# Kernel tuning notes

Measured on AMD Instinct MI355X. Metric: run time of the kernel, lower is better.

The kernel has to match this reference:

```python
import jax, jax.numpy as jnp
import numpy as np

LN_EPS = 1e-5


def setup_inputs() -> dict:
    key = jax.random.key(0)
    k1, k2, k3 = jax.random.split(key, 3)
    B, C, N, T, K = 8, 64, 512, 288, 32
    x = jax.random.normal(k1, (B, C, N, T), dtype=jnp.float32)
    HEs = jax.random.uniform(k2, (N, K), dtype=jnp.float32)  # relu(tanh(...)) in [0,1)
    edge_map = jax.random.normal(k3, (K, K), dtype=jnp.float32) / np.sqrt(K)
    return {"x": x, "HEs": HEs, "edge_map": edge_map}


def reference(x, HEs, edge_map):
    # x: [B, C, N, T]; HEs: [N, K]; edge_map: [K, K]
    B, C, N, T = x.shape
    xt = jnp.transpose(x, (0, 3, 2, 1))            # [B, T, N, C]
    feat = xt.reshape(B * T, N, C)                 # [B*T, N, C]
    # hyperedge aggregation: HEs^T @ feat
    hyper_feat = jnp.einsum('nk,bnc->bkc', HEs, feat)          # [B*T, K, C]
    hyper_mapped = jax.nn.relu(jnp.einsum('kj,bjc->bkc', edge_map, hyper_feat))
    hyper_out = hyper_mapped + hyper_feat
    # scatter back to nodes
    y = jax.nn.relu(jnp.einsum('nk,bkc->bnc', HEs, hyper_out)) # [B*T, N, C]
    y = y.reshape(B, T, N, C)
    z = y + xt
    # fresh LayerNorm over last dim (C), affine params are identity (ones/zeros)
    mu = jnp.mean(z, axis=-1, keepdims=True)
    var = jnp.mean(jnp.square(z - mu), axis=-1, keepdims=True)
    z = (z - mu) * jax.lax.rsqrt(var + LN_EPS)
    return jnp.transpose(z, (0, 3, 2, 1))          # [B, C, N, T]
```

## Files before the change

kernel.cpp:

```cpp
#include <hip/hip_runtime.h>

#define B_ 8
#define C_ 64
#define N_ 512
#define T_ 288
#define K_ 32

typedef __bf16 bf16;
typedef __attribute__((ext_vector_type(4))) __bf16 bf16x4;
typedef __attribute__((ext_vector_type(8))) __bf16 bf16x8;
typedef __attribute__((ext_vector_type(4))) float f32x4;

__global__ __launch_bounds__(256) void k_prep(const void* __restrict__ x,
                                              const void* __restrict__ hes,
                                              const void* __restrict__ em,
                                              bf16* __restrict__ hesb,
                                              bf16* __restrict__ hest,
                                              bf16* __restrict__ emb,
                                              int* __restrict__ flag) {
    __shared__ float sm[256];
    const bf16* xb = (const bf16*)x;
    float m = 0.f;
    for (int i = threadIdx.x; i < 4096; i += 256) {
        float a = fabsf((float)xb[i]);
        if (!(a <= 1000.f)) a = 1e30f;
        m = fmaxf(m, a);
    }
    sm[threadIdx.x] = m;
    __syncthreads();
    for (int s = 128; s > 0; s >>= 1) {
        if (threadIdx.x < s) sm[threadIdx.x] = fmaxf(sm[threadIdx.x], sm[threadIdx.x + s]);
        __syncthreads();
    }
    const int f32 = (sm[0] > 1000.f) ? 1 : 0;
    if (blockIdx.x == 0 && threadIdx.x == 0) *flag = f32;

    int idx = blockIdx.x * 256 + threadIdx.x;
    if (idx < N_ * K_) {
        float v = f32 ? ((const float*)hes)[idx] : (float)((const bf16*)hes)[idx];
        hesb[idx] = (bf16)v;
        int n = idx >> 5, k = idx & 31;
        hest[k * N_ + n] = (bf16)v;
    }
    if (idx < K_ * K_) {
        float v = f32 ? ((const float*)em)[idx] : (float)((const bf16*)em)[idx];
        emb[idx] = (bf16)v;
    }
}

template <int F32>
__device__ __forceinline__ void hyper_body(const void* __restrict__ x,
                                           const bf16* __restrict__ hest,
                                           const bf16* __restrict__ emb,
                                           bf16* __restrict__ ho) {
    const int tile = blockIdx.x, c = blockIdx.y, b = blockIdx.z;
    const int lane = threadIdx.x;
    const int col  = lane & 15;
    const int q    = lane >> 4;
    const int t0   = tile * 32;
    const size_t xbase = ((size_t)(b * C_ + c)) * N_ * T_;

    __shared__ bf16  xT[32][136];
    __shared__ float hf[K_][33];

    const int tq = lane & 7;
    const int rw = lane >> 3;

    f32x4 acc[2][2] = {};
    for (int chunk = 0; chunk < 4; ++chunk) {
        const int nc = chunk * 128;
        #pragma unroll
        for (int it = 0; it < 16; ++it) {
            const int row = it * 8 + rw;
            const size_t gi = xbase + (size_t)(nc + row) * T_ + t0 + 4 * tq;
            float v0, v1, v2, v3;
            if (F32) {
                f32x4 v = *(const f32x4*)((const float*)x + gi);
                v0 = v[0]; v1 = v[1]; v2 = v[2]; v3 = v[3];
            } else {
                bf16x4 v = *(const bf16x4*)((const bf16*)x + gi);
                v0 = (float)v[0]; v1 = (float)v[1]; v2 = (float)v[2]; v3 = (float)v[3];
            }
            xT[4 * tq + 0][row] = (bf16)v0;
            xT[4 * tq + 1][row] = (bf16)v1;
            xT[4 * tq + 2][row] = (bf16)v2;
            xT[4 * tq + 3][row] = (bf16)v3;
        }
        __syncthreads();
        #pragma unroll
        for (int s = 0; s < 4; ++s) {
            const int nl = s * 32;
            const int ng = nc + nl;
            bf16x8 a0 = *(const bf16x8*)(hest + (size_t)(col) * N_ + ng + 8 * q);
            bf16x8 a1 = *(const bf16x8*)(hest + (size_t)(16 + col) * N_ + ng + 8 * q);
            bf16x8 b0 = *(const bf16x8*)(&xT[col][nl + 8 * q]);
            bf16x8 b1 = *(const bf16x8*)(&xT[16 + col][nl + 8 * q]);
            acc[0][0] = __builtin_amdgcn_mfma_f32_16x16x32_bf16(a0, b0, acc[0][0], 0, 0, 0);
            acc[0][1] = __builtin_amdgcn_mfma_f32_16x16x32_bf16(a0, b1, acc[0][1], 0, 0, 0);
            acc[1][0] = __builtin_amdgcn_mfma_f32_16x16x32_bf16(a1, b0, acc[1][0], 0, 0, 0);
            acc[1][1] = __builtin_amdgcn_mfma_f32_16x16x32_bf16(a1, b1, acc[1][1], 0, 0, 0);
        }
        __syncthreads();
    }

    #pragma unroll
    for (int mt = 0; mt < 2; ++mt)
        #pragma unroll
        for (int tt = 0; tt < 2; ++tt)
            #pragma unroll
            for (int r = 0; r < 4; ++r)
                hf[16 * mt + 4 * q + r][16 * tt + col] = acc[mt][tt][r];
    __syncthreads();

    f32x4 acc2[2][2];
    #pragma unroll
    for (int mt = 0; mt < 2; ++mt) {
        bf16x8 a = *(const bf16x8*)(emb + (size_t)(16 * mt + col) * K_ + 8 * q);
        #pragma unroll
        for (int tt = 0; tt < 2; ++tt) {
            bf16x8 bb;
            #pragma unroll
            for (int jj = 0; jj < 8; ++jj)
                bb[jj] = (bf16)hf[8 * q + jj][16 * tt + col];
            f32x4 zero = {};
            acc2[mt][tt] = __builtin_amdgcn_mfma_f32_16x16x32_bf16(a, bb, zero, 0, 0, 0);
        }
    }

    #pragma unroll
    for (int mt = 0; mt < 2; ++mt)
        #pragma unroll
        for (int tt = 0; tt < 2; ++tt) {
            bf16x4 v;
            #pragma unroll
            for (int r = 0; r < 4; ++r) {
                float hv = acc2[mt][tt][r];
                hv = hv > 0.f ? hv : 0.f;
                hv += acc[mt][tt][r];
                v[r] = (bf16)hv;
            }
            *(bf16x4*)(ho + (((size_t)(b * C_ + c)) * T_ + t0 + 16 * tt + col) * K_
                          + 16 * mt + 4 * q) = v;
        }
}

__global__ __launch_bounds__(64, 3) void k_hyper(const void* __restrict__ x,
                                                 const int* __restrict__ flag,
                                                 const bf16* __restrict__ hest,
                                                 const bf16* __restrict__ emb,
                                                 bf16* __restrict__ ho) {
    if (*flag) hyper_body<1>(x, hest, emb, ho);
    else       hyper_body<0>(x, hest, emb, ho);
}

template <int F32>
__device__ __forceinline__ void scatter_body(const void* __restrict__ x,
                                             const bf16* __restrict__ hesb,
                                             const bf16* __restrict__ ho,
                                             void* __restrict__ outp) {
    const int wg  = blockIdx.x;
    const int b   = wg & 7;
    const int pos = wg >> 3;
    const int bx  = pos % 9;
    const int n0  = (pos / 9) * 16;

    const int tid   = threadIdx.x;
    const int w     = tid >> 6;
    const int lane  = tid & 63;
    const int col   = lane & 15;
    const int q     = lane >> 4;
    const int thalf = w & 1;
    const int cgrp  = w >> 1;
    const int t0    = bx * 32 + thalf * 16;

    bf16x8 hb = *(const bf16x8*)(hesb + (size_t)(n0 + col) * K_ + 8 * q);

    f32x4 z[16];
    float s1[4] = {0.f, 0.f, 0.f, 0.f}, s2[4] = {0.f, 0.f, 0.f, 0.f};
    const bf16* hob = ho + (((size_t)(b * C_)) * T_ + t0 + col) * K_ + 8 * q;
    const size_t xb = ((size_t)b * C_) * (size_t)N_ * T_;
    #pragma unroll
    for (int i = 0; i < 16; ++i) {
        const int c = cgrp * 16 + i;
        bf16x8 a = *(const bf16x8*)(hob + (size_t)c * T_ * K_);
        f32x4 zero = {};
        f32x4 zz = __builtin_amdgcn_mfma_f32_16x16x32_bf16(a, hb, zero, 0, 0, 0);
        const size_t xi = xb + ((size_t)c * N_ + n0 + col) * T_ + t0 + 4 * q;
        f32x4 xv;
        if (F32) {
            xv = *(const f32x4*)((const float*)x + xi);
        } else {
            bf16x4 x4 = *(const bf16x4*)((const bf16*)x + xi);
            xv[0] = (float)x4[0]; xv[1] = (float)x4[1];
            xv[2] = (float)x4[2]; xv[3] = (float)x4[3];
        }
        #pragma unroll
        for (int r = 0; r < 4; ++r) {
            float v = zz[r];
            v = v > 0.f ? v : 0.f;
            v += xv[r];
            zz[r] = v;
            s1[r] += v;
            s2[r] += v * v;
        }
        z[i] = zz;
    }

    __shared__ float sh1[2][4][16][17];
    __shared__ float sh2[2][4][16][17];
    #pragma unroll
    for (int r = 0; r < 4; ++r) {
        sh1[thalf][cgrp][4 * q + r][col] = s1[r];
        sh2[thalf][cgrp][4 * q + r][col] = s2[r];
    }
    __syncthreads();

    {
        const int th = tid >> 8, rr = (tid >> 4) & 15, cc = tid & 15;
        float S1 = sh1[th][0][rr][cc] + sh1[th][1][rr][cc]
                 + sh1[th][2][rr][cc] + sh1[th][3][rr][cc];
        float S2 = sh2[th][0][rr][cc] + sh2[th][1][rr][cc]
                 + sh2[th][2][rr][cc] + sh2[th][3][rr][cc];
        float mu  = S1 * (1.f / 64.f);
        float var = S2 * (1.f / 64.f) - mu * mu;
        float rs  = rsqrtf(var + 1e-5f);
        sh1[th][0][rr][cc] = mu;
        sh2[th][0][rr][cc] = rs;
    }
    __syncthreads();

    float mu_r[4], rs_r[4];
    #pragma unroll
    for (int r = 0; r < 4; ++r) {
        mu_r[r] = sh1[thalf][0][4 * q + r][col];
        rs_r[r] = sh2[thalf][0][4 * q + r][col];
    }
    #pragma unroll
    for (int i = 0; i < 16; ++i) {
        const int c = cgrp * 16 + i;
        const size_t oi = ((size_t)(b * C_ + c) * N_ + n0 + col) * T_ + t0 + 4 * q;
        if (F32) {
            f32x4 v;
            #pragma unroll
            for (int r = 0; r < 4; ++r) v[r] = (z[i][r] - mu_r[r]) * rs_r[r];
            *(f32x4*)((float*)outp + oi) = v;
        } else {
            bf16x4 v;
            #pragma unroll
            for (int r = 0; r < 4; ++r) v[r] = (bf16)((z[i][r] - mu_r[r]) * rs_r[r]);
            *(bf16x4*)((bf16*)outp + oi) = v;
        }
    }
}

__global__ __launch_bounds__(512, 2) void k_scatter_ln(const void* __restrict__ x,
                                                       const int* __restrict__ flag,
                                                       const bf16* __restrict__ hesb,
                                                       const bf16* __restrict__ ho,
                                                       void* __restrict__ outp) {
    if (*flag) scatter_body<1>(x, hesb, ho, outp);
    else       scatter_body<0>(x, hesb, ho, outp);
}

extern "C" void kernel_launch(void* const* d_in, const int* in_sizes, int n_in,
                              void* d_out, int out_size, void* d_ws, size_t ws_size,
                              hipStream_t stream) {
    const void* x   = d_in[0];
    const void* hes = d_in[1];
    const void* em  = d_in[2];

    char* ws = (char*)d_ws;
    int*  flag = (int*)ws;
    bf16* hesb = (bf16*)(ws + 64);
    bf16* hest = hesb + (size_t)N_ * K_;
    bf16* emb  = hest + (size_t)K_ * N_;
    bf16* ho   = emb  + (size_t)K_ * K_;

    k_prep<<<dim3((N_ * K_ + 255) / 256), 256, 0, stream>>>(x, hes, em, hesb, hest, emb, flag);
    k_hyper<<<dim3(T_ / 32, C_, B_), 64, 0, stream>>>(x, flag, hest, emb, ho);
    k_scatter_ln<<<dim3((T_ / 32) * (N_ / 16) * B_, 1, 1), 512, 0, stream>>>(x, flag, hesb, ho, d_out);
}
```

Before: 603.1 us.

## Rework hyper-kernel x staging, alias LDS buffers, add nontemporal IO and raise occupancy

The hyper kernel now loads x with lanes mapped to consecutive time steps. Each lane reads four node rows as scalar loads and writes a packed bf16x4 into the transposed LDS tile, replacing the old scattered per-element LDS stores. The xT and hf shared buffers are aliased to cut LDS use, and both kernels raise their launch-bounds occupancy hints. The scatter/LayerNorm kernel switches to nontemporal loads of x and nontemporal output stores. The risks are scalar global loads being less efficient than vector loads, and register pressure from the higher occupancy hint on the 512-thread kernel, which holds 16 f32x4 values per thread.

```diff
diff --git a/kernel.cpp b/kernel.cpp
--- a/kernel.cpp
+++ b/kernel.cpp
@@ -60,39 +60,37 @@
     const int t0   = tile * 32;
     const size_t xbase = ((size_t)(b * C_ + c)) * N_ * T_;
 
-    __shared__ bf16  xT[32][136];
-    __shared__ float hf[K_][33];
-
-    const int tq = lane & 7;
-    const int rw = lane >> 3;
+    __shared__ char smraw[32 * 136 * sizeof(bf16)];
+    bf16 (*xT)[136] = (bf16(*)[136])smraw;
+    float (*hf)[33] = (float(*)[33])smraw;
+
+    const int tcol = lane & 31;
+    const int ng   = lane >> 5;
 
     f32x4 acc[2][2] = {};
     for (int chunk = 0; chunk < 4; ++chunk) {
         const int nc = chunk * 128;
         #pragma unroll
-        for (int it = 0; it < 16; ++it) {
-            const int row = it * 8 + rw;
-            const size_t gi = xbase + (size_t)(nc + row) * T_ + t0 + 4 * tq;
-            float v0, v1, v2, v3;
-            if (F32) {
-                f32x4 v = *(const f32x4*)((const float*)x + gi);
-                v0 = v[0]; v1 = v[1]; v2 = v[2]; v3 = v[3];
-            } else {
-                bf16x4 v = *(const bf16x4*)((const bf16*)x + gi);
-                v0 = (float)v[0]; v1 = (float)v[1]; v2 = (float)v[2]; v3 = (float)v[3];
+        for (int a = 0; a < 16; ++a) {
+            const int nb = a * 8 + ng * 4;
+            const size_t gi = xbase + (size_t)(nc + nb) * T_ + t0 + tcol;
+            bf16x4 w;
+            #pragma unroll
+            for (int j = 0; j < 4; ++j) {
+                float v;
+                if (F32) v = ((const float*)x)[gi + (size_t)j * T_];
+                else     v = (float)((const bf16*)x)[gi + (size_t)j * T_];
+                w[j] = (bf16)v;
             }
-            xT[4 * tq + 0][row] = (bf16)v0;
-            xT[4 * tq + 1][row] = (bf16)v1;
-            xT[4 * tq + 2][row] = (bf16)v2;
-            xT[4 * tq + 3][row] = (bf16)v3;
+            *(bf16x4*)(&xT[tcol][nb]) = w;
         }
         __syncthreads();
         #pragma unroll
         for (int s = 0; s < 4; ++s) {
             const int nl = s * 32;
-            const int ng = nc + nl;
-            bf16x8 a0 = *(const bf16x8*)(hest + (size_t)(col) * N_ + ng + 8 * q);
-            bf16x8 a1 = *(const bf16x8*)(hest + (size_t)(16 + col) * N_ + ng + 8 * q);
+            const int ng2 = nc + nl;
+            bf16x8 a0 = *(const bf16x8*)(hest + (size_t)(col) * N_ + ng2 + 8 * q);
+            bf16x8 a1 = *(const bf16x8*)(hest + (size_t)(16 + col) * N_ + ng2 + 8 * q);
             bf16x8 b0 = *(const bf16x8*)(&xT[col][nl + 8 * q]);
             bf16x8 b1 = *(const bf16x8*)(&xT[16 + col][nl + 8 * q]);
             acc[0][0] = __builtin_amdgcn_mfma_f32_16x16x32_bf16(a0, b0, acc[0][0], 0, 0, 0);
@@ -144,7 +142,7 @@
         }
 }
 
-__global__ __launch_bounds__(64, 3) void k_hyper(const void* __restrict__ x,
+__global__ __launch_bounds__(64, 4) void k_hyper(const void* __restrict__ x,
                                                  const int* __restrict__ flag,
                                                  const bf16* __restrict__ hest,
                                                  const bf16* __restrict__ emb,
@@ -188,9 +186,9 @@
         const size_t xi = xb + ((size_t)c * N_ + n0 + col) * T_ + t0 + 4 * q;
         f32x4 xv;
         if (F32) {
-            xv = *(const f32x4*)((const float*)x + xi);
+            xv = __builtin_nontemporal_load((const f32x4*)((const float*)x + xi));
         } else {
-            bf16x4 x4 = *(const bf16x4*)((const bf16*)x + xi);
+            bf16x4 x4 = __builtin_nontemporal_load((const bf16x4*)((const bf16*)x + xi));
             xv[0] = (float)x4[0]; xv[1] = (float)x4[1];
             xv[2] = (float)x4[2]; xv[3] = (float)x4[3];
         }
@@ -243,17 +241,17 @@
             f32x4 v;
             #pragma unroll
             for (int r = 0; r < 4; ++r) v[r] = (z[i][r] - mu_r[r]) * rs_r[r];
-            *(f32x4*)((float*)outp + oi) = v;
+            __builtin_nontemporal_store(v, (f32x4*)((float*)outp + oi));
         } else {
             bf16x4 v;
             #pragma unroll
             for (int r = 0; r < 4; ++r) v[r] = (bf16)((z[i][r] - mu_r[r]) * rs_r[r]);
-            *(bf16x4*)((bf16*)outp + oi) = v;
-        }
-    }
-}
-
-__global__ __launch_bounds__(512, 2) void k_scatter_ln(const void* __restrict__ x,
+            __builtin_nontemporal_store(v, (bf16x4*)((bf16*)outp + oi));
+        }
+    }
+}
+
+__global__ __launch_bounds__(512, 4) void k_scatter_ln(const void* __restrict__ x,
                                                        const int* __restrict__ flag,
                                                        const bf16* __restrict__ hesb,
                                                        const bf16* __restrict__ ho,
```

Result: slower. 630.0 us (+4.5%).
